# Performance work log

Measured on AMD Instinct MI355X. Metric: run time of the kernel, lower is better.

Reference implementation:

```python
import jax, jax.numpy as jnp
import numpy as np

B, S, D, H = 4, 1024, 1024, 16
HD = D // H  # head_dim = 64


def setup_inputs() -> dict:
    key = jax.random.key(0)
    ks = jax.random.split(key, 12)
    scale = 1.0 / np.sqrt(D)
    inp = {
        "query": jax.random.normal(ks[0], (B, S, D), jnp.float32),
        "key": jax.random.normal(ks[1], (B, S, D), jnp.float32),
        "value": jax.random.normal(ks[2], (B, S, D), jnp.float32),
        "mask": jnp.zeros((B, S), dtype=bool),  # accepted but unused by the module
        "Wq": jax.random.normal(ks[3], (D, D), jnp.float32) * scale,
        "bq": jnp.zeros((D,), jnp.float32),
        "Wk": jax.random.normal(ks[4], (D, D), jnp.float32) * scale,
        "bk": jnp.zeros((D,), jnp.float32),
        "Wv": jax.random.normal(ks[5], (D, D), jnp.float32) * scale,
        "bv": jnp.zeros((D,), jnp.float32),
        "Wo": jax.random.normal(ks[6], (D, D), jnp.float32) * scale,
        "bo": jnp.zeros((D,), jnp.float32),
    }
    return inp


def _split_heads(x):
    # [B,S,D] -> [B,H,S,HD]
    b, s, _ = x.shape
    return x.reshape(b, s, H, HD).transpose(0, 2, 1, 3)


def reference(query, key, value, mask, Wq, bq, Wk, bk, Wv, bv, Wo, bo):
    b, s, _ = query.shape
    q = _split_heads(query @ Wq.T + bq)
    k = _split_heads(key @ Wk.T + bk)
    v = _split_heads(value @ Wv.T + bv)
    # dense scores, then hollow mask: triu(diag=1) and tril(diag=-1) are both
    # filled with -inf, leaving ONLY the diagonal unmasked
    scores = jnp.einsum("bhqd,bhkd->bhqk", q, k) / jnp.sqrt(jnp.float32(HD))
    diag = jnp.eye(s, dtype=bool)  # the only surviving positions
    scores = jnp.where(diag, scores, -jnp.inf)
    attn = jax.nn.softmax(scores, axis=-1)  # == identity one-hot rows
    out = jnp.einsum("bhqk,bhkd->bhqd", attn, v)
    out = out.transpose(0, 2, 1, 3).reshape(b, s, H * HD)
    return out @ Wo.T + bo
```

## Files before the change

### kernel.cpp

```cpp
#include <hip/hip_runtime.h>
#include <stdint.h>


typedef __attribute__((ext_vector_type(4))) float f32x4;
typedef __attribute__((ext_vector_type(8))) __bf16 bf16x8;
typedef __attribute__((ext_vector_type(4))) float float4v;
typedef __attribute__((ext_vector_type(8))) unsigned short ushort8;
typedef __attribute__((ext_vector_type(4))) unsigned short us4;

#define DEVINL __device__ __forceinline__

DEVINL unsigned short f2bf(float f) {
  union { float f; uint32_t u; } c; c.f = f;
  uint32_t r = c.u + 0x7FFFu + ((c.u >> 16) & 1u);
  return (unsigned short)(r >> 16);
}

#define GLD16(g, l) __builtin_amdgcn_global_load_lds( \
    (__attribute__((address_space(1))) void*)(g),     \
    (__attribute__((address_space(3))) void*)(l), 16, 0, 0)

__global__ __launch_bounds__(256) void convert_v_wo(
    const float* __restrict__ V, const float* __restrict__ Wo,
    unsigned short* __restrict__ Vb, unsigned short* __restrict__ Wob) {
  const long NV = 4194304;
  long idx = ((long)blockIdx.x * 256 + threadIdx.x) * 8;
  const float* src; unsigned short* dst; long off;
  if (idx < NV) { src = V; dst = Vb; off = idx; }
  else          { src = Wo; dst = Wob; off = idx - NV; }
  float4v a = *(const float4v*)(src + off);
  float4v b = *(const float4v*)(src + off + 4);
  ushort8 o;
  o[0]=f2bf(a[0]); o[1]=f2bf(a[1]); o[2]=f2bf(a[2]); o[3]=f2bf(a[3]);
  o[4]=f2bf(b[0]); o[5]=f2bf(b[1]); o[6]=f2bf(b[2]); o[7]=f2bf(b[3]);
  *(ushort8*)(dst + off) = o;
}

__global__ __launch_bounds__(256) void transp_wv(
    const float* __restrict__ Wv, unsigned short* __restrict__ WvT) {
  __shared__ unsigned short tile[64][65];
  const int c0 = (blockIdx.x & 15) * 64;
  const int j0 = (blockIdx.x >> 4) * 64;
  const int t = threadIdx.x;
  const int tr = t >> 4;
  const int tc = (t & 15) * 4;
  #pragma unroll
  for (int rr = 0; rr < 4; ++rr) {
    int row = tr + rr * 16;
    float4v v = *(const float4v*)(Wv + (long)(j0 + row) * 1024 + c0 + tc);
    tile[row][tc+0] = f2bf(v[0]);
    tile[row][tc+1] = f2bf(v[1]);
    tile[row][tc+2] = f2bf(v[2]);
    tile[row][tc+3] = f2bf(v[3]);
  }
  __syncthreads();
  #pragma unroll
  for (int rr = 0; rr < 4; ++rr) {
    int crow = tr + rr * 16;
    us4 o;
    #pragma unroll
    for (int i = 0; i < 4; ++i) o[i] = tile[tc + i][crow];
    *(us4*)(WvT + (long)(c0 + crow) * 1024 + j0 + tc) = o;
  }
}

__global__ __launch_bounds__(256) void bias2_kernel(
    const float* __restrict__ Wo, const float* __restrict__ bv,
    const float* __restrict__ bo, float* __restrict__ bias2) {
  const int w = threadIdx.x >> 6, lane = threadIdx.x & 63;
  const int row = blockIdx.x * 4 + w;
  float s = 0.f;
  #pragma unroll
  for (int c = 0; c < 4; ++c) {
    int col = c * 256 + lane * 4;
    float4v a = *(const float4v*)(Wo + (long)row * 1024 + col);
    float4v b = *(const float4v*)(bv + col);
    s += a[0]*b[0] + a[1]*b[1] + a[2]*b[2] + a[3]*b[3];
  }
  #pragma unroll
  for (int off = 32; off; off >>= 1) s += __shfl_down(s, off);
  if (lane == 0) bias2[row] = s + bo[row];
}

template<int OUT_BF16, int ADD_BIAS>
__global__ __launch_bounds__(512) void gemm_nt(
    const unsigned short* __restrict__ A,
    const unsigned short* __restrict__ B,
    const float* __restrict__ bias,
    void* __restrict__ Cv) {
  constexpr int K = 1024, N = 1024;
  __shared__ alignas(16) unsigned short lA[128 * 64];
  __shared__ alignas(16) unsigned short lB[128 * 64];

  const int t = threadIdx.x;
  const int bm = blockIdx.x >> 3;
  const int bn = blockIdx.x & 7;
  const int m0 = bm << 7, n0 = bn << 7;

  const int srow = t >> 3;
  const int swz = (t & 7) ^ (srow & 7);
  const unsigned short* gA0 = A + (long)(m0 + srow) * K + swz * 8;
  const unsigned short* gB0 = B + (long)(n0 + srow) * K + swz * 8;
  unsigned short* lA0 = lA + t * 8;
  unsigned short* lB0 = lB + t * 8;

  const int lane = t & 63;
  const int wr = t >> 8;
  const int wc = (t >> 6) & 3;
  const int fr = lane & 15;
  const int fq = lane >> 4;

  int aoff[4][2], boff[2][2];
  #pragma unroll
  for (int m = 0; m < 4; ++m) {
    int row = wr * 64 + m * 16 + fr;
    #pragma unroll
    for (int h = 0; h < 2; ++h)
      aoff[m][h] = row * 128 + (((h * 4 + fq) ^ (row & 7)) * 16);
  }
  #pragma unroll
  for (int n = 0; n < 2; ++n) {
    int row = wc * 32 + n * 16 + fr;
    #pragma unroll
    for (int h = 0; h < 2; ++h)
      boff[n][h] = row * 128 + (((h * 4 + fq) ^ (row & 7)) * 16);
  }

  f32x4 acc[4][2] = {};
  const char* lAb = (const char*)lA;
  const char* lBb = (const char*)lB;

  #pragma unroll 1
  for (int kt = 0; kt < K / 64; ++kt) {
    __syncthreads();
    const unsigned short* ga = gA0 + kt * 64;
    const unsigned short* gb = gB0 + kt * 64;
    GLD16(ga, lA0);
    GLD16(ga + 64 * K, lA0 + 4096);
    GLD16(gb, lB0);
    GLD16(gb + 64 * K, lB0 + 4096);
    __syncthreads();

    bf16x8 av[4][2], bw[2][2];
    #pragma unroll
    for (int m = 0; m < 4; ++m)
      #pragma unroll
      for (int h = 0; h < 2; ++h)
        av[m][h] = *(const bf16x8*)(lAb + aoff[m][h]);
    #pragma unroll
    for (int n = 0; n < 2; ++n)
      #pragma unroll
      for (int h = 0; h < 2; ++h)
        bw[n][h] = *(const bf16x8*)(lBb + boff[n][h]);

    #pragma unroll
    for (int m = 0; m < 4; ++m)
      #pragma unroll
      for (int n = 0; n < 2; ++n)
        #pragma unroll
        for (int h = 0; h < 2; ++h)
          acc[m][n] = __builtin_amdgcn_mfma_f32_16x16x32_bf16(
              av[m][h], bw[n][h], acc[m][n], 0, 0, 0);
  }

  #pragma unroll
  for (int m = 0; m < 4; ++m) {
    #pragma unroll
    for (int n = 0; n < 2; ++n) {
      int gr = m0 + wr * 64 + m * 16 + fq * 4;
      int gc = n0 + wc * 32 + n * 16 + fr;
      float bb = 0.f;
      if (ADD_BIAS) bb = bias[gc];
      if (OUT_BF16) {
        unsigned short* C = (unsigned short*)Cv;
        #pragma unroll
        for (int j = 0; j < 4; ++j)
          C[(long)(gr + j) * N + gc] = f2bf(acc[m][n][j] + bb);
      } else {
        float* C = (float*)Cv;
        #pragma unroll
        for (int j = 0; j < 4; ++j)
          C[(long)(gr + j) * N + gc] = acc[m][n][j] + bb;
      }
    }
  }
}

extern "C" void kernel_launch(void* const* d_in, const int* in_sizes, int n_in,
                              void* d_out, int out_size, void* d_ws, size_t ws_size,
                              hipStream_t stream) {
  const float* value = (const float*)d_in[2];
  const float* Wv    = (const float*)d_in[8];
  const float* bv    = (const float*)d_in[9];
  const float* Wo    = (const float*)d_in[10];
  const float* bo    = (const float*)d_in[11];

  char* ws = (char*)d_ws;
  unsigned short* Vb    = (unsigned short*)(ws);
  unsigned short* Wob   = (unsigned short*)(ws + 8388608);
  unsigned short* WvTb  = (unsigned short*)(ws + 10485760);
  unsigned short* Wb    = (unsigned short*)(ws + 12582912);
  float*          bias2 = (float*)(ws + 14680064);
  float* out = (float*)d_out;

  convert_v_wo<<<2560, 256, 0, stream>>>(value, Wo, Vb, Wob);
  transp_wv<<<256, 256, 0, stream>>>(Wv, WvTb);
  bias2_kernel<<<256, 256, 0, stream>>>(Wo, bv, bo, bias2);
  gemm_nt<1, 0><<<64, 512, 0, stream>>>(Wob, WvTb, nullptr, Wb);
  gemm_nt<0, 1><<<256, 512, 0, stream>>>(Vb, Wb, bias2, out);
}
```

Measured before the change: 153.0 us.

## Fuse prep kernels, double-buffer GEMM LDS loads, and retile GEMMs for more blocks

Merges the three preprocessing kernels (bf16 conversion of V and Wo, the Wv transpose, and the bias fold) into one launch dispatched by block index. The GEMM is templated on tile shape and double-buffers its LDS tiles so the global-to-LDS loads for the next K step are issued before the current step's MFMAs. The two GEMMs use smaller tiles (64x64 and 128x64) to launch 256 and 512 blocks instead of 64 and 256, which fills more of the GPU's compute units. In exchange it uses twice the LDS per block and gives less reuse per tile. The loop has a single barrier per iteration, so whether the prefetch writes are properly ordered against the wait on outstanding loads is unclear.

```diff
diff --git a/kernel.cpp b/kernel.cpp
--- a/kernel.cpp
+++ b/kernel.cpp
@@ -20,155 +20,172 @@
     (__attribute__((address_space(1))) void*)(g),     \
     (__attribute__((address_space(3))) void*)(l), 16, 0, 0)
 
-__global__ __launch_bounds__(256) void convert_v_wo(
-    const float* __restrict__ V, const float* __restrict__ Wo,
-    unsigned short* __restrict__ Vb, unsigned short* __restrict__ Wob) {
-  const long NV = 4194304;
-  long idx = ((long)blockIdx.x * 256 + threadIdx.x) * 8;
-  const float* src; unsigned short* dst; long off;
-  if (idx < NV) { src = V; dst = Vb; off = idx; }
-  else          { src = Wo; dst = Wob; off = idx - NV; }
-  float4v a = *(const float4v*)(src + off);
-  float4v b = *(const float4v*)(src + off + 4);
-  ushort8 o;
-  o[0]=f2bf(a[0]); o[1]=f2bf(a[1]); o[2]=f2bf(a[2]); o[3]=f2bf(a[3]);
-  o[4]=f2bf(b[0]); o[5]=f2bf(b[1]); o[6]=f2bf(b[2]); o[7]=f2bf(b[3]);
-  *(ushort8*)(dst + off) = o;
-}
-
-__global__ __launch_bounds__(256) void transp_wv(
-    const float* __restrict__ Wv, unsigned short* __restrict__ WvT) {
+__global__ __launch_bounds__(256) void prep(
+    const float* __restrict__ V, const float* __restrict__ Wv,
+    const float* __restrict__ Wo, const float* __restrict__ bv,
+    const float* __restrict__ bo,
+    unsigned short* __restrict__ Vb, unsigned short* __restrict__ Wob,
+    unsigned short* __restrict__ WvT, float* __restrict__ bias2) {
   __shared__ unsigned short tile[64][65];
-  const int c0 = (blockIdx.x & 15) * 64;
-  const int j0 = (blockIdx.x >> 4) * 64;
-  const int t = threadIdx.x;
-  const int tr = t >> 4;
-  const int tc = (t & 15) * 4;
-  #pragma unroll
-  for (int rr = 0; rr < 4; ++rr) {
-    int row = tr + rr * 16;
-    float4v v = *(const float4v*)(Wv + (long)(j0 + row) * 1024 + c0 + tc);
-    tile[row][tc+0] = f2bf(v[0]);
-    tile[row][tc+1] = f2bf(v[1]);
-    tile[row][tc+2] = f2bf(v[2]);
-    tile[row][tc+3] = f2bf(v[3]);
-  }
-  __syncthreads();
-  #pragma unroll
-  for (int rr = 0; rr < 4; ++rr) {
-    int crow = tr + rr * 16;
-    us4 o;
-    #pragma unroll
-    for (int i = 0; i < 4; ++i) o[i] = tile[tc + i][crow];
-    *(us4*)(WvT + (long)(c0 + crow) * 1024 + j0 + tc) = o;
-  }
-}
-
-__global__ __launch_bounds__(256) void bias2_kernel(
-    const float* __restrict__ Wo, const float* __restrict__ bv,
-    const float* __restrict__ bo, float* __restrict__ bias2) {
-  const int w = threadIdx.x >> 6, lane = threadIdx.x & 63;
-  const int row = blockIdx.x * 4 + w;
-  float s = 0.f;
-  #pragma unroll
-  for (int c = 0; c < 4; ++c) {
-    int col = c * 256 + lane * 4;
-    float4v a = *(const float4v*)(Wo + (long)row * 1024 + col);
-    float4v b = *(const float4v*)(bv + col);
-    s += a[0]*b[0] + a[1]*b[1] + a[2]*b[2] + a[3]*b[3];
-  }
-  #pragma unroll
-  for (int off = 32; off; off >>= 1) s += __shfl_down(s, off);
-  if (lane == 0) bias2[row] = s + bo[row];
-}
-
-template<int OUT_BF16, int ADD_BIAS>
-__global__ __launch_bounds__(512) void gemm_nt(
+  const int b = blockIdx.x, t = threadIdx.x;
+  if (b < 2560) {
+    const float* src = (b < 2048) ? V : Wo;
+    unsigned short* dst = (b < 2048) ? Vb : Wob;
+    long off = ((long)(b < 2048 ? b : b - 2048) * 256 + t) * 8;
+    float4v a = *(const float4v*)(src + off);
+    float4v c = *(const float4v*)(src + off + 4);
+    ushort8 o;
+    o[0]=f2bf(a[0]); o[1]=f2bf(a[1]); o[2]=f2bf(a[2]); o[3]=f2bf(a[3]);
+    o[4]=f2bf(c[0]); o[5]=f2bf(c[1]); o[6]=f2bf(c[2]); o[7]=f2bf(c[3]);
+    *(ushort8*)(dst + off) = o;
+  } else if (b < 2816) {
+    const int tb = b - 2560;
+    const int c0 = (tb & 15) * 64, j0 = (tb >> 4) * 64;
+    const int tr = t >> 4, tc = (t & 15) * 4;
+    #pragma unroll
+    for (int rr = 0; rr < 4; ++rr) {
+      int row = tr + rr * 16;
+      float4v v = *(const float4v*)(Wv + (long)(j0 + row) * 1024 + c0 + tc);
+      tile[row][tc+0] = f2bf(v[0]);
+      tile[row][tc+1] = f2bf(v[1]);
+      tile[row][tc+2] = f2bf(v[2]);
+      tile[row][tc+3] = f2bf(v[3]);
+    }
+    __syncthreads();
+    #pragma unroll
+    for (int rr = 0; rr < 4; ++rr) {
+      int crow = tr + rr * 16;
+      us4 o;
+      #pragma unroll
+      for (int i = 0; i < 4; ++i) o[i] = tile[tc + i][crow];
+      *(us4*)(WvT + (long)(c0 + crow) * 1024 + j0 + tc) = o;
+    }
+  } else {
+    const int tb = b - 2816;
+    const int w = t >> 6, lane = t & 63;
+    const int row = tb * 4 + w;
+    float s = 0.f;
+    #pragma unroll
+    for (int c = 0; c < 4; ++c) {
+      int col = c * 256 + lane * 4;
+      float4v a = *(const float4v*)(Wo + (long)row * 1024 + col);
+      float4v x = *(const float4v*)(bv + col);
+      s += a[0]*x[0] + a[1]*x[1] + a[2]*x[2] + a[3]*x[3];
+    }
+    #pragma unroll
+    for (int off = 32; off; off >>= 1) s += __shfl_down(s, off);
+    if (lane == 0) bias2[row] = s + bo[row];
+  }
+}
+
+template<int BM, int BN, int NT, int WM, int WN, int OUT_BF16, int ADD_BIAS>
+__global__ __launch_bounds__(NT) void gemm_nt(
     const unsigned short* __restrict__ A,
     const unsigned short* __restrict__ B,
     const float* __restrict__ bias,
     void* __restrict__ Cv) {
   constexpr int K = 1024, N = 1024;
-  __shared__ alignas(16) unsigned short lA[128 * 64];
-  __shared__ alignas(16) unsigned short lB[128 * 64];
+  constexpr int NBN = N / BN;
+  constexpr int SM = BM / WM, SN = BN / WN;
+  constexpr int FM = SM / 16, FN = SN / 16;
+  constexpr int CA = BM * 8 / NT, CB = BN * 8 / NT;
+  constexpr int NKT = K / 64;
+
+  __shared__ alignas(16) unsigned short lA[2][BM * 64];
+  __shared__ alignas(16) unsigned short lB[2][BN * 64];
 
   const int t = threadIdx.x;
-  const int bm = blockIdx.x >> 3;
-  const int bn = blockIdx.x & 7;
-  const int m0 = bm << 7, n0 = bn << 7;
-
-  const int srow = t >> 3;
-  const int swz = (t & 7) ^ (srow & 7);
-  const unsigned short* gA0 = A + (long)(m0 + srow) * K + swz * 8;
-  const unsigned short* gB0 = B + (long)(n0 + srow) * K + swz * 8;
-  unsigned short* lA0 = lA + t * 8;
-  unsigned short* lB0 = lB + t * 8;
+  const int bm = blockIdx.x / NBN;
+  const int bn = blockIdx.x % NBN;
+  const int m0 = bm * BM, n0 = bn * BN;
+
+  long gAoff[CA]; int lAoff[CA];
+  #pragma unroll
+  for (int c = 0; c < CA; ++c) {
+    int s = c * NT + t, r = s >> 3, sl = (s & 7) ^ (r & 7);
+    gAoff[c] = (long)(m0 + r) * K + sl * 8;
+    lAoff[c] = s * 8;
+  }
+  long gBoff[CB]; int lBoff[CB];
+  #pragma unroll
+  for (int c = 0; c < CB; ++c) {
+    int s = c * NT + t, r = s >> 3, sl = (s & 7) ^ (r & 7);
+    gBoff[c] = (long)(n0 + r) * K + sl * 8;
+    lBoff[c] = s * 8;
+  }
 
   const int lane = t & 63;
-  const int wr = t >> 8;
-  const int wc = (t >> 6) & 3;
-  const int fr = lane & 15;
-  const int fq = lane >> 4;
-
-  int aoff[4][2], boff[2][2];
-  #pragma unroll
-  for (int m = 0; m < 4; ++m) {
-    int row = wr * 64 + m * 16 + fr;
+  const int w = t >> 6, wm = w / WN, wn = w % WN;
+  const int fr = lane & 15, fq = lane >> 4;
+
+  int aoff[FM][2], boff[FN][2];
+  #pragma unroll
+  for (int m = 0; m < FM; ++m) {
+    int row = wm * SM + m * 16 + fr;
     #pragma unroll
     for (int h = 0; h < 2; ++h)
       aoff[m][h] = row * 128 + (((h * 4 + fq) ^ (row & 7)) * 16);
   }
   #pragma unroll
-  for (int n = 0; n < 2; ++n) {
-    int row = wc * 32 + n * 16 + fr;
+  for (int n = 0; n < FN; ++n) {
+    int row = wn * SN + n * 16 + fr;
     #pragma unroll
     for (int h = 0; h < 2; ++h)
       boff[n][h] = row * 128 + (((h * 4 + fq) ^ (row & 7)) * 16);
   }
 
-  f32x4 acc[4][2] = {};
-  const char* lAb = (const char*)lA;
-  const char* lBb = (const char*)lB;
-
+  f32x4 acc[FM][FN] = {};
+
+  #pragma unroll
+  for (int c = 0; c < CA; ++c) GLD16(A + gAoff[c], (unsigned short*)lA[0] + lAoff[c]);
+  #pragma unroll
+  for (int c = 0; c < CB; ++c) GLD16(B + gBoff[c], (unsigned short*)lB[0] + lBoff[c]);
+  __syncthreads();
+
+  int cur = 0;
   #pragma unroll 1
-  for (int kt = 0; kt < K / 64; ++kt) {
-    __syncthreads();
-    const unsigned short* ga = gA0 + kt * 64;
-    const unsigned short* gb = gB0 + kt * 64;
-    GLD16(ga, lA0);
-    GLD16(ga + 64 * K, lA0 + 4096);
-    GLD16(gb, lB0);
-    GLD16(gb + 64 * K, lB0 + 4096);
-    __syncthreads();
-
-    bf16x8 av[4][2], bw[2][2];
-    #pragma unroll
-    for (int m = 0; m < 4; ++m)
+  for (int kt = 0; kt < NKT; ++kt) {
+    if (kt + 1 < NKT) {
+      #pragma unroll
+      for (int c = 0; c < CA; ++c)
+        GLD16(A + gAoff[c] + (kt + 1) * 64, (unsigned short*)lA[cur ^ 1] + lAoff[c]);
+      #pragma unroll
+      for (int c = 0; c < CB; ++c)
+        GLD16(B + gBoff[c] + (kt + 1) * 64, (unsigned short*)lB[cur ^ 1] + lBoff[c]);
+    }
+    const char* lAb = (const char*)lA[cur];
+    const char* lBb = (const char*)lB[cur];
+    bf16x8 av[FM][2], bw[FN][2];
+    #pragma unroll
+    for (int m = 0; m < FM; ++m)
       #pragma unroll
       for (int h = 0; h < 2; ++h)
         av[m][h] = *(const bf16x8*)(lAb + aoff[m][h]);
     #pragma unroll
-    for (int n = 0; n < 2; ++n)
+    for (int n = 0; n < FN; ++n)
       #pragma unroll
       for (int h = 0; h < 2; ++h)
         bw[n][h] = *(const bf16x8*)(lBb + boff[n][h]);
 
     #pragma unroll
-    for (int m = 0; m < 4; ++m)
-      #pragma unroll
-      for (int n = 0; n < 2; ++n)
+    for (int m = 0; m < FM; ++m)
+      #pragma unroll
+      for (int n = 0; n < FN; ++n)
         #pragma unroll
         for (int h = 0; h < 2; ++h)
           acc[m][n] = __builtin_amdgcn_mfma_f32_16x16x32_bf16(
               av[m][h], bw[n][h], acc[m][n], 0, 0, 0);
-  }
-
-  #pragma unroll
-  for (int m = 0; m < 4; ++m) {
-    #pragma unroll
-    for (int n = 0; n < 2; ++n) {
-      int gr = m0 + wr * 64 + m * 16 + fq * 4;
-      int gc = n0 + wc * 32 + n * 16 + fr;
+
+    __syncthreads();
+    cur ^= 1;
+  }
+
+  #pragma unroll
+  for (int m = 0; m < FM; ++m) {
+    #pragma unroll
+    for (int n = 0; n < FN; ++n) {
+      int gr = m0 + wm * SM + m * 16 + fq * 4;
+      int gc = n0 + wn * SN + n * 16 + fr;
       float bb = 0.f;
       if (ADD_BIAS) bb = bias[gc];
       if (OUT_BF16) {
@@ -203,9 +220,7 @@
   float*          bias2 = (float*)(ws + 14680064);
   float* out = (float*)d_out;
 
-  convert_v_wo<<<2560, 256, 0, stream>>>(value, Wo, Vb, Wob);
-  transp_wv<<<256, 256, 0, stream>>>(Wv, WvTb);
-  bias2_kernel<<<256, 256, 0, stream>>>(Wo, bv, bo, bias2);
-  gemm_nt<1, 0><<<64, 512, 0, stream>>>(Wob, WvTb, nullptr, Wb);
-  gemm_nt<0, 1><<<256, 512, 0, stream>>>(Vb, Wb, bias2, out);
-}
+  prep<<<3072, 256, 0, stream>>>(value, Wv, Wo, bv, bo, Vb, Wob, WvTb, bias2);
+  gemm_nt<64, 64, 512, 2, 4, 1, 0><<<256, 512, 0, stream>>>(Wob, WvTb, nullptr, Wb);
+  gemm_nt<128, 64, 512, 4, 2, 0, 1><<<512, 512, 0, stream>>>(Vb, Wb, bias2, out);
+}
```

Measured after the change: 139.0 us. 1.1x faster.
